# Optimization experiments

Hardware: AMD Instinct MI355X
Metric: run time of the kernel (lower is better)

Reference implementation:

```python
import jax, jax.numpy as jnp
import numpy as np

FEATURE_DIM = 2048
LABEL_DIM = 80
EMBED_DIM = 512
OUTPUT_DIM = 2048
NUM_EXPERTS = 8
BATCH = 1024
IN_DIM = FEATURE_DIM + EMBED_DIM


def setup_inputs() -> dict:
    key = jax.random.key(0)
    ks = jax.random.split(key, 7)
    features = jax.random.normal(ks[0], (BATCH, FEATURE_DIM), dtype=jnp.float32)
    labels = jax.random.uniform(ks[1], (BATCH, LABEL_DIM), dtype=jnp.float32)
    # learned parameters
    label_embed = jax.random.normal(ks[2], (LABEL_DIM, EMBED_DIM), dtype=jnp.float32)
    gate_w = jax.random.normal(ks[3], (IN_DIM, NUM_EXPERTS), dtype=jnp.float32) * (1.0 / np.sqrt(IN_DIM))
    gate_b = jnp.zeros((NUM_EXPERTS,), dtype=jnp.float32)
    expert_w = jax.random.normal(ks[4], (NUM_EXPERTS, IN_DIM, OUTPUT_DIM), dtype=jnp.float32) * (1.0 / np.sqrt(IN_DIM))
    expert_b = jnp.zeros((NUM_EXPERTS, OUTPUT_DIM), dtype=jnp.float32)
    return {
        "features": features,
        "labels": labels,
        "label_embed": label_embed,
        "gate_w": gate_w,
        "gate_b": gate_b,
        "expert_w": expert_w,
        "expert_b": expert_b,
    }


def reference(features, labels, label_embed, gate_w, gate_b, expert_w, expert_b):
    # labels: [B, L] soft multilabel -> label embedding mix [B, E]
    label_embeds = labels @ label_embed                      # [B, EMBED_DIM]
    combined = jnp.concatenate([features, label_embeds], axis=-1)  # [B, IN_DIM]
    gating = jax.nn.sigmoid(combined @ gate_w + gate_b)      # [B, NUM_EXPERTS]
    # all-experts batched GEMM: [B, IN] x [E, IN, OUT] -> [B, E, OUT]
    expert_out = jnp.einsum('bi,eio->beo', combined, expert_w) + expert_b[None, :, :]
    # gate-weighted reduction over experts
    out = jnp.einsum('be,beo->bo', gating, expert_out)       # [B, OUT]
    return out
```

## Files before the change

kernel.cpp:

```cpp
#include <hip/hip_runtime.h>
#include <hip/hip_bf16.h>

#define BATCH   1024
#define FDIM    2048
#define LDIM    80
#define EDIM    512
#define ODIM    2048
#define NEXP    8
#define INDIM   2560

#define BM      256
#define BN      256
#define BK      64
#define NKT     (INDIM / BK)

typedef __bf16 bf16x8 __attribute__((ext_vector_type(8)));
typedef float  f32x4  __attribute__((ext_vector_type(4)));

__device__ __forceinline__ unsigned int pack2(float lo, float hi) {
    __hip_bfloat162 h = __float22bfloat162_rn(make_float2(lo, hi));
    unsigned int u;
    __builtin_memcpy(&u, &h, 4);
    return u;
}
__device__ __forceinline__ float bf2f(unsigned short h) {
    return __uint_as_float((unsigned int)h << 16);
}
__device__ __forceinline__ void gload_lds16(const void* g, void* l) {
    __builtin_amdgcn_global_load_lds(
        (__attribute__((address_space(1))) void*)g,
        (__attribute__((address_space(3))) void*)l,
        16, 0, 0);
}

#define BAR()       __builtin_amdgcn_s_barrier()
#define SCHED_PIN() __builtin_amdgcn_sched_barrier(0)

__global__ __launch_bounds__(256) void convert_w(
    const float* __restrict__ W, unsigned short* __restrict__ Wb)
{
    const int t  = threadIdx.x;
    const int o  = blockIdx.x * 256 + t;
    const int k0 = blockIdx.y * 32;
    const int e  = blockIdx.z;
    const float* src = W + (size_t)e * ((size_t)INDIM * ODIM) + (size_t)k0 * ODIM + o;
    unsigned int pk[16];
    #pragma unroll
    for (int j = 0; j < 16; ++j) {
        float a = src[(size_t)(2 * j) * ODIM];
        float b = src[(size_t)(2 * j + 1) * ODIM];
        pk[j] = pack2(a, b);
    }
    uint4* dst = (uint4*)(Wb + (size_t)e * ((size_t)ODIM * INDIM) + (size_t)o * INDIM + k0);
    dst[0] = make_uint4(pk[0],  pk[1],  pk[2],  pk[3]);
    dst[1] = make_uint4(pk[4],  pk[5],  pk[6],  pk[7]);
    dst[2] = make_uint4(pk[8],  pk[9],  pk[10], pk[11]);
    dst[3] = make_uint4(pk[12], pk[13], pk[14], pk[15]);
}

__global__ __launch_bounds__(256) void prep_kernel(
    const float* __restrict__ features, const float* __restrict__ labels,
    const float* __restrict__ label_embed, unsigned short* __restrict__ cb)
{
    const int b0 = blockIdx.x * 4;
    const int t  = threadIdx.x;
    __shared__ float lab[4][LDIM];
    for (int idx = t; idx < 4 * LDIM; idx += 256) {
        lab[idx / LDIM][idx % LDIM] = labels[(size_t)(b0 + idx / LDIM) * LDIM + (idx % LDIM)];
    }
    __syncthreads();

    {
        const int r = t >> 6, c64 = t & 63;
        const float4* F4 = (const float4*)features;
        #pragma unroll
        for (int ch = 0; ch < 8; ++ch) {
            float4 v = F4[(size_t)(b0 + r) * (FDIM / 4) + c64 + 64 * ch];
            uint2 pk;
            pk.x = pack2(v.x, v.y);
            pk.y = pack2(v.z, v.w);
            *(uint2*)(cb + (size_t)(b0 + r) * INDIM + (size_t)(c64 + 64 * ch) * 4) = pk;
        }
    }
    {
        const int j = 2 * t;
        float acc[4][2] = {{0,0},{0,0},{0,0},{0,0}};
        const float2* le2 = (const float2*)label_embed;
        for (int l = 0; l < LDIM; ++l) {
            float2 le = le2[(size_t)l * (EDIM / 2) + t];
            #pragma unroll
            for (int r = 0; r < 4; ++r) {
                float lv = lab[r][l];
                acc[r][0] += lv * le.x;
                acc[r][1] += lv * le.y;
            }
        }
        #pragma unroll
        for (int r = 0; r < 4; ++r) {
            *(unsigned int*)(cb + (size_t)(b0 + r) * INDIM + FDIM + j) = pack2(acc[r][0], acc[r][1]);
        }
    }
}

__global__ __launch_bounds__(256) void gate_kernel(
    const unsigned short* __restrict__ cb, const float* __restrict__ gw,
    const float* __restrict__ gb, float* __restrict__ gating)
{
    const int b = blockIdx.x, t = threadIdx.x;
    float p[NEXP] = {0,0,0,0,0,0,0,0};
    for (int i = t; i < INDIM; i += 256) {
        float c = bf2f(cb[(size_t)b * INDIM + i]);
        const float4* g4 = (const float4*)(gw + (size_t)i * NEXP);
        float4 u = g4[0], v = g4[1];
        p[0] += c * u.x; p[1] += c * u.y; p[2] += c * u.z; p[3] += c * u.w;
        p[4] += c * v.x; p[5] += c * v.y; p[6] += c * v.z; p[7] += c * v.w;
    }
    __shared__ float red[4][NEXP];
    const int lane = t & 63, wave = t >> 6;
    #pragma unroll
    for (int e = 0; e < NEXP; ++e) {
        float v = p[e];
        v += __shfl_down(v, 32); v += __shfl_down(v, 16); v += __shfl_down(v, 8);
        v += __shfl_down(v, 4);  v += __shfl_down(v, 2);  v += __shfl_down(v, 1);
        if (lane == 0) red[wave][e] = v;
    }
    __syncthreads();
    if (t < NEXP) {
        float s = red[0][t] + red[1][t] + red[2][t] + red[3][t] + gb[t];
        gating[(size_t)b * NEXP + t] = 1.0f / (1.0f + __expf(-s));
    }
}

__global__ __launch_bounds__(512, 2) void moe_gemm8(
    const unsigned short* __restrict__ cb, const unsigned short* __restrict__ Wb,
    const float* __restrict__ gating, const float* __restrict__ eb,
    float* __restrict__ out)
{
    __shared__ unsigned short smem[2 * 2 * 256 * 64];

    const int t = threadIdx.x;
    const int lane = t & 63, wave = t >> 6;
    const int n0 = blockIdx.x * BN;
    const int m0 = blockIdx.y * BM;
    const int e  = blockIdx.z;

    const int wmi = wave >> 2;
    const int wni = wave & 3;
    const int wmBase = wmi * 128;
    const int wnBase = wni * 64;
    const int fm = lane & 15, fq = lane >> 4;
    const int fsw = fm & 7;

    const int srow = t >> 3;
    const int scn  = (t & 7) ^ (srow & 7);
    const size_t gOff = (size_t)srow * INDIM + (size_t)scn * 8;
    const unsigned short* aS = cb + (size_t)m0 * INDIM + gOff;
    const unsigned short* bS = Wb + (size_t)e * ((size_t)ODIM * INDIM)
                                  + (size_t)n0 * INDIM + gOff;

    #define STAGE_A(p, q, kt) gload_lds16(aS + (size_t)(q) * (64 * INDIM) + (size_t)(kt) * 64, \
            smem + (((p) * 2 + 0) * 256 + (q) * 64) * 64 + wave * 512)
    #define STAGE_B(p, q, kt) gload_lds16(bS + (size_t)(q) * (64 * INDIM) + (size_t)(kt) * 64, \
            smem + (((p) * 2 + 1) * 256 + (q) * 64) * 64 + wave * 512)

    f32x4 acc[8][4];
    #pragma unroll
    for (int i = 0; i < 8; ++i)
        #pragma unroll
        for (int j = 0; j < 4; ++j) acc[i][j] = (f32x4){0.f, 0.f, 0.f, 0.f};

    bf16x8 af[4][2], bA[2][2], bB[2][2];

    STAGE_A(0, 0, 0); STAGE_A(0, 2, 0); STAGE_B(0, 0, 0); STAGE_B(0, 1, 0);
    STAGE_B(0, 2, 0); STAGE_B(0, 3, 0); STAGE_A(0, 1, 0); STAGE_A(0, 3, 0);
    STAGE_A(1, 0, 1); STAGE_A(1, 2, 1); STAGE_B(1, 0, 1); STAGE_B(1, 1, 1);
    STAGE_B(1, 2, 1); STAGE_B(1, 3, 1);
    asm volatile("s_waitcnt vmcnt(6)");
    BAR();

    for (int kt = 0; kt < NKT; ++kt) {
        const int p  = kt & 1;
        const int np = p ^ 1;
        const unsigned short* Ac = smem + (p * 2 + 0) * (256 * 64);
        const unsigned short* Bc = smem + (p * 2 + 1) * (256 * 64);

        #pragma unroll
        for (int mi = 0; mi < 4; ++mi)
            #pragma unroll
            for (int ks = 0; ks < 2; ++ks)
                af[mi][ks] = *(const bf16x8*)(Ac + (wmBase + mi * 16 + fm) * 64
                                                 + (((ks * 4 + fq) ^ fsw) * 8));
        #pragma unroll
        for (int ni = 0; ni < 2; ++ni)
            #pragma unroll
            for (int ks = 0; ks < 2; ++ks)
                bA[ni][ks] = *(const bf16x8*)(Bc + (wnBase + ni * 16 + fm) * 64
                                                 + (((ks * 4 + fq) ^ fsw) * 8));
        if (kt + 1 < NKT) { STAGE_A(np, 1, kt + 1); STAGE_A(np, 3, kt + 1); }
        BAR();
        __builtin_amdgcn_s_setprio(1);
        #pragma unroll
        for (int mi = 0; mi < 4; ++mi)
            #pragma unroll
            for (int ni = 0; ni < 2; ++ni)
                #pragma unroll
                for (int ks = 0; ks < 2; ++ks)
                    acc[mi][ni] = __builtin_amdgcn_mfma_f32_16x16x32_bf16(
                        af[mi][ks], bA[ni][ks], acc[mi][ni], 0, 0, 0);
        __builtin_amdgcn_s_setprio(0);
        SCHED_PIN();
        BAR();

        #pragma unroll
        for (int ni = 0; ni < 2; ++ni)
            #pragma unroll
            for (int ks = 0; ks < 2; ++ks)
                bB[ni][ks] = *(const bf16x8*)(Bc + (wnBase + (2 + ni) * 16 + fm) * 64
                                                 + (((ks * 4 + fq) ^ fsw) * 8));
        if (kt + 2 < NKT) { STAGE_A(p, 0, kt + 2); STAGE_A(p, 2, kt + 2); }
        BAR();
        __builtin_amdgcn_s_setprio(1);
        #pragma unroll
        for (int mi = 0; mi < 4; ++mi)
            #pragma unroll
            for (int ni = 0; ni < 2; ++ni)
                #pragma unroll
                for (int ks = 0; ks < 2; ++ks)
                    acc[mi][2 + ni] = __builtin_amdgcn_mfma_f32_16x16x32_bf16(
                        af[mi][ks], bB[ni][ks], acc[mi][2 + ni], 0, 0, 0);
        __builtin_amdgcn_s_setprio(0);
        SCHED_PIN();
        BAR();

        #pragma unroll
        for (int mi = 0; mi < 4; ++mi)
            #pragma unroll
            for (int ks = 0; ks < 2; ++ks)
                af[mi][ks] = *(const bf16x8*)(Ac + (wmBase + 64 + mi * 16 + fm) * 64
                                                 + (((ks * 4 + fq) ^ fsw) * 8));
        if (kt + 2 < NKT) { STAGE_B(p, 0, kt + 2); STAGE_B(p, 1, kt + 2); }
        BAR();
        __builtin_amdgcn_s_setprio(1);
        #pragma unroll
        for (int mi = 0; mi < 4; ++mi)
            #pragma unroll
            for (int ni = 0; ni < 2; ++ni)
                #pragma unroll
                for (int ks = 0; ks < 2; ++ks)
                    acc[4 + mi][2 + ni] = __builtin_amdgcn_mfma_f32_16x16x32_bf16(
                        af[mi][ks], bB[ni][ks], acc[4 + mi][2 + ni], 0, 0, 0);
        __builtin_amdgcn_s_setprio(0);
        SCHED_PIN();
        BAR();

        if (kt + 2 < NKT) { STAGE_B(p, 2, kt + 2); STAGE_B(p, 3, kt + 2); }
        BAR();
        __builtin_amdgcn_s_setprio(1);
        #pragma unroll
        for (int mi = 0; mi < 4; ++mi)
            #pragma unroll
            for (int ni = 0; ni < 2; ++ni)
                #pragma unroll
                for (int ks = 0; ks < 2; ++ks)
                    acc[4 + mi][ni] = __builtin_amdgcn_mfma_f32_16x16x32_bf16(
                        af[mi][ks], bA[ni][ks], acc[4 + mi][ni], 0, 0, 0);
        __builtin_amdgcn_s_setprio(0);
        SCHED_PIN();
        if (kt + 2 < NKT) { asm volatile("s_waitcnt vmcnt(6)"); }
        else              { asm volatile("s_waitcnt vmcnt(0)"); }
        BAR();
    }
    #undef STAGE_A
    #undef STAGE_B

    #pragma unroll
    for (int mi = 0; mi < 8; ++mi) {
        const int grow = m0 + wmBase + mi * 16 + fq * 4;
        const float g0 = gating[(size_t)(grow + 0) * NEXP + e];
        const float g1 = gating[(size_t)(grow + 1) * NEXP + e];
        const float g2 = gating[(size_t)(grow + 2) * NEXP + e];
        const float g3 = gating[(size_t)(grow + 3) * NEXP + e];
        #pragma unroll
        for (int ni = 0; ni < 4; ++ni) {
            const int gcol = n0 + wnBase + ni * 16 + fm;
            const float bias = eb[(size_t)e * ODIM + gcol];
            f32x4 a = acc[mi][ni];
            unsafeAtomicAdd(out + (size_t)(grow + 0) * ODIM + gcol, g0 * (a.x + bias));
            unsafeAtomicAdd(out + (size_t)(grow + 1) * ODIM + gcol, g1 * (a.y + bias));
            unsafeAtomicAdd(out + (size_t)(grow + 2) * ODIM + gcol, g2 * (a.z + bias));
            unsafeAtomicAdd(out + (size_t)(grow + 3) * ODIM + gcol, g3 * (a.w + bias));
        }
    }
}

__global__ __launch_bounds__(256) void moe_gemm_slow(
    const unsigned short* __restrict__ cb, const float* __restrict__ W,
    const float* __restrict__ gating, const float* __restrict__ eb,
    float* __restrict__ out)
{
    __shared__ unsigned short As[128 * 32];
    __shared__ unsigned short Bs[128 * 32];

    const int t = threadIdx.x;
    const int lane = t & 63, wave = t >> 6;
    const int n0 = blockIdx.x * 128;
    const int m0 = blockIdx.y * 128;
    const int e  = blockIdx.z;

    f32x4 acc[4][4];
    #pragma unroll
    for (int i = 0; i < 4; ++i)
        #pragma unroll
        for (int j = 0; j < 4; ++j) acc[i][j] = (f32x4){0.f, 0.f, 0.f, 0.f};

    const int arow = t >> 2, acg = t & 3;
    const unsigned short* ag0 = cb + (size_t)(m0 + arow) * INDIM + acg * 8;
    unsigned short* al0 = As + wave * 512;
    unsigned short* al1 = As + 2048 + wave * 512;

    const int bg = t & 15;
    const int bu = t >> 4;
    const float* wg = W + (size_t)e * ((size_t)INDIM * ODIM) + (size_t)(2 * bg) * ODIM + n0 + bu * 8;
    unsigned int* bl = (unsigned int*)Bs + bg + bu * 128;

    const int fm = lane & 15, fq = lane >> 4;
    const int wn = (wave & 1) * 64;
    const int wm = (wave >> 1) * 64;

    for (int k0 = 0; k0 < INDIM; k0 += 32) {
        __syncthreads();
        gload_lds16(ag0 + k0, al0);
        gload_lds16(ag0 + (size_t)64 * INDIM + k0, al1);
        const float* wp = wg + (size_t)k0 * ODIM;
        float4 r0a = *(const float4*)(wp);
        float4 r0b = *(const float4*)(wp + 4);
        float4 r1a = *(const float4*)(wp + ODIM);
        float4 r1b = *(const float4*)(wp + ODIM + 4);
        bl[0 * 16] = pack2(r0a.x, r1a.x);
        bl[1 * 16] = pack2(r0a.y, r1a.y);
        bl[2 * 16] = pack2(r0a.z, r1a.z);
        bl[3 * 16] = pack2(r0a.w, r1a.w);
        bl[4 * 16] = pack2(r0b.x, r1b.x);
        bl[5 * 16] = pack2(r0b.y, r1b.y);
        bl[6 * 16] = pack2(r0b.z, r1b.z);
        bl[7 * 16] = pack2(r0b.w, r1b.w);
        __syncthreads();

        bf16x8 af[4], bfr[4];
        #pragma unroll
        for (int mi = 0; mi < 4; ++mi)
            af[mi] = *(const bf16x8*)(As + (wm + mi * 16 + fm) * 32 + fq * 8);
        #pragma unroll
        for (int ni = 0; ni < 4; ++ni)
            bfr[ni] = *(const bf16x8*)(Bs + (wn + ni * 16 + fm) * 32 + fq * 8);
        #pragma unroll
        for (int mi = 0; mi < 4; ++mi)
            #pragma unroll
            for (int ni = 0; ni < 4; ++ni)
                acc[mi][ni] = __builtin_amdgcn_mfma_f32_16x16x32_bf16(af[mi], bfr[ni], acc[mi][ni], 0, 0, 0);
    }

    #pragma unroll
    for (int mi = 0; mi < 4; ++mi) {
        const int grow = m0 + wm + mi * 16 + fq * 4;
        const float g0 = gating[(size_t)(grow + 0) * NEXP + e];
        const float g1 = gating[(size_t)(grow + 1) * NEXP + e];
        const float g2 = gating[(size_t)(grow + 2) * NEXP + e];
        const float g3 = gating[(size_t)(grow + 3) * NEXP + e];
        #pragma unroll
        for (int ni = 0; ni < 4; ++ni) {
            const int gcol = n0 + wn + ni * 16 + fm;
            const float bias = eb[(size_t)e * ODIM + gcol];
            f32x4 a = acc[mi][ni];
            unsafeAtomicAdd(out + (size_t)(grow + 0) * ODIM + gcol, g0 * (a.x + bias));
            unsafeAtomicAdd(out + (size_t)(grow + 1) * ODIM + gcol, g1 * (a.y + bias));
            unsafeAtomicAdd(out + (size_t)(grow + 2) * ODIM + gcol, g2 * (a.z + bias));
            unsafeAtomicAdd(out + (size_t)(grow + 3) * ODIM + gcol, g3 * (a.w + bias));
        }
    }
}

extern "C" void kernel_launch(void* const* d_in, const int* in_sizes, int n_in,
                              void* d_out, int out_size, void* d_ws, size_t ws_size,
                              hipStream_t stream) {
    const float* features    = (const float*)d_in[0];
    const float* labels      = (const float*)d_in[1];
    const float* label_embed = (const float*)d_in[2];
    const float* gate_w      = (const float*)d_in[3];
    const float* gate_b      = (const float*)d_in[4];
    const float* expert_w    = (const float*)d_in[5];
    const float* expert_b    = (const float*)d_in[6];
    float* out = (float*)d_out;

    const size_t wb_bytes = (size_t)NEXP * ODIM * INDIM * 2;
    const size_t cb_bytes = (size_t)BATCH * INDIM * 2;
    const size_t gt_bytes = (size_t)BATCH * NEXP * 4;
    const bool fast = ws_size >= wb_bytes + cb_bytes + gt_bytes;

    hipMemsetAsync(d_out, 0, (size_t)BATCH * ODIM * sizeof(float), stream);

    if (fast) {
        unsigned short* Wb = (unsigned short*)d_ws;
        unsigned short* cb = (unsigned short*)((char*)d_ws + wb_bytes);
        float* gating = (float*)((char*)d_ws + wb_bytes + cb_bytes);
        convert_w<<<dim3(ODIM / 256, INDIM / 32, NEXP), 256, 0, stream>>>(expert_w, Wb);
        prep_kernel<<<BATCH / 4, 256, 0, stream>>>(features, labels, label_embed, cb);
        gate_kernel<<<BATCH, 256, 0, stream>>>(cb, gate_w, gate_b, gating);
        moe_gemm8<<<dim3(ODIM / BN, BATCH / BM, NEXP), 512, 0, stream>>>(cb, Wb, gating, expert_b, out);
    } else {
        unsigned short* cb = (unsigned short*)d_ws;
        float* gating = (float*)((char*)d_ws + cb_bytes);
        prep_kernel<<<BATCH / 4, 256, 0, stream>>>(features, labels, label_embed, cb);
        gate_kernel<<<BATCH, 256, 0, stream>>>(cb, gate_w, gate_b, gating);
        moe_gemm_slow<<<dim3(ODIM / 128, BATCH / 128, NEXP), 256, 0, stream>>>(cb, expert_w, gating, expert_b, out);
    }
}
```

Baseline: 426.8 us.

## Split LDS buffers and unroll the K loop by two with a reworked prefetch schedule

Replaces the single indexed shared-memory array with four named A/B ping-pong buffers. The K loop is unrolled by two so buffer selection happens at compile time instead of through runtime parity math. The prefetch schedule also changes: each tile now loads all of next tile's A in one burst at the start, and B two tiles ahead after the last B read, replacing the interleaved half-tile staging. The aim is less address arithmetic and simpler vmcnt accounting, at the risk of burstier global loads and different latency overlap.

```diff
diff --git a/kernel.cpp b/kernel.cpp
--- a/kernel.cpp
+++ b/kernel.cpp
@@ -136,7 +136,10 @@
     const float* __restrict__ gating, const float* __restrict__ eb,
     float* __restrict__ out)
 {
-    __shared__ unsigned short smem[2 * 2 * 256 * 64];
+    __shared__ unsigned short As0[256 * 64];
+    __shared__ unsigned short Bs0[256 * 64];
+    __shared__ unsigned short As1[256 * 64];
+    __shared__ unsigned short Bs1[256 * 64];
 
     const int t = threadIdx.x;
     const int lane = t & 63, wave = t >> 6;
@@ -158,10 +161,26 @@
     const unsigned short* bS = Wb + (size_t)e * ((size_t)ODIM * INDIM)
                                   + (size_t)n0 * INDIM + gOff;
 
-    #define STAGE_A(p, q, kt) gload_lds16(aS + (size_t)(q) * (64 * INDIM) + (size_t)(kt) * 64, \
-            smem + (((p) * 2 + 0) * 256 + (q) * 64) * 64 + wave * 512)
-    #define STAGE_B(p, q, kt) gload_lds16(bS + (size_t)(q) * (64 * INDIM) + (size_t)(kt) * 64, \
-            smem + (((p) * 2 + 1) * 256 + (q) * 64) * 64 + wave * 512)
+    #define STAGE4_A(DST, kt) { _Pragma("unroll") for (int q = 0; q < 4; ++q) \
+        gload_lds16(aS + (size_t)q * (64 * INDIM) + (size_t)(kt) * 64, (DST) + q * 4096 + wave * 512); }
+    #define STAGE4_B(DST, kt) { _Pragma("unroll") for (int q = 0; q < 4; ++q) \
+        gload_lds16(bS + (size_t)q * (64 * INDIM) + (size_t)(kt) * 64, (DST) + q * 4096 + wave * 512); }
+
+    #define PH_READ_A(RA, base) { _Pragma("unroll") for (int mi = 0; mi < 4; ++mi) \
+        _Pragma("unroll") for (int ks = 0; ks < 2; ++ks) \
+            af[mi][ks] = *(const bf16x8*)((RA) + (wmBase + (base) + mi * 16 + fm) * 64 \
+                                               + (((ks * 4 + fq) ^ fsw) * 8)); }
+    #define PH_READ_B(BF, RB, base) { _Pragma("unroll") for (int ni = 0; ni < 2; ++ni) \
+        _Pragma("unroll") for (int ks = 0; ks < 2; ++ks) \
+            BF[ni][ks] = *(const bf16x8*)((RB) + (wnBase + (base) + ni * 16 + fm) * 64 \
+                                               + (((ks * 4 + fq) ^ fsw) * 8)); }
+    #define MFMA16(AI, AJ, BF) { __builtin_amdgcn_s_setprio(1); \
+        _Pragma("unroll") for (int mi = 0; mi < 4; ++mi) \
+        _Pragma("unroll") for (int ni = 0; ni < 2; ++ni) \
+        _Pragma("unroll") for (int ks = 0; ks < 2; ++ks) \
+            acc[(AI) + mi][(AJ) + ni] = __builtin_amdgcn_mfma_f32_16x16x32_bf16( \
+                af[mi][ks], BF[ni][ks], acc[(AI) + mi][(AJ) + ni], 0, 0, 0); \
+        __builtin_amdgcn_s_setprio(0); }
 
     f32x4 acc[8][4];
     #pragma unroll
@@ -171,107 +190,48 @@
 
     bf16x8 af[4][2], bA[2][2], bB[2][2];
 
-    STAGE_A(0, 0, 0); STAGE_A(0, 2, 0); STAGE_B(0, 0, 0); STAGE_B(0, 1, 0);
-    STAGE_B(0, 2, 0); STAGE_B(0, 3, 0); STAGE_A(0, 1, 0); STAGE_A(0, 3, 0);
-    STAGE_A(1, 0, 1); STAGE_A(1, 2, 1); STAGE_B(1, 0, 1); STAGE_B(1, 1, 1);
-    STAGE_B(1, 2, 1); STAGE_B(1, 3, 1);
-    asm volatile("s_waitcnt vmcnt(6)");
-    BAR();
-
-    for (int kt = 0; kt < NKT; ++kt) {
-        const int p  = kt & 1;
-        const int np = p ^ 1;
-        const unsigned short* Ac = smem + (p * 2 + 0) * (256 * 64);
-        const unsigned short* Bc = smem + (p * 2 + 1) * (256 * 64);
-
-        #pragma unroll
-        for (int mi = 0; mi < 4; ++mi)
-            #pragma unroll
-            for (int ks = 0; ks < 2; ++ks)
-                af[mi][ks] = *(const bf16x8*)(Ac + (wmBase + mi * 16 + fm) * 64
-                                                 + (((ks * 4 + fq) ^ fsw) * 8));
-        #pragma unroll
-        for (int ni = 0; ni < 2; ++ni)
-            #pragma unroll
-            for (int ks = 0; ks < 2; ++ks)
-                bA[ni][ks] = *(const bf16x8*)(Bc + (wnBase + ni * 16 + fm) * 64
-                                                 + (((ks * 4 + fq) ^ fsw) * 8));
-        if (kt + 1 < NKT) { STAGE_A(np, 1, kt + 1); STAGE_A(np, 3, kt + 1); }
-        BAR();
-        __builtin_amdgcn_s_setprio(1);
-        #pragma unroll
-        for (int mi = 0; mi < 4; ++mi)
-            #pragma unroll
-            for (int ni = 0; ni < 2; ++ni)
-                #pragma unroll
-                for (int ks = 0; ks < 2; ++ks)
-                    acc[mi][ni] = __builtin_amdgcn_mfma_f32_16x16x32_bf16(
-                        af[mi][ks], bA[ni][ks], acc[mi][ni], 0, 0, 0);
-        __builtin_amdgcn_s_setprio(0);
-        SCHED_PIN();
-        BAR();
-
-        #pragma unroll
-        for (int ni = 0; ni < 2; ++ni)
-            #pragma unroll
-            for (int ks = 0; ks < 2; ++ks)
-                bB[ni][ks] = *(const bf16x8*)(Bc + (wnBase + (2 + ni) * 16 + fm) * 64
-                                                 + (((ks * 4 + fq) ^ fsw) * 8));
-        if (kt + 2 < NKT) { STAGE_A(p, 0, kt + 2); STAGE_A(p, 2, kt + 2); }
-        BAR();
-        __builtin_amdgcn_s_setprio(1);
-        #pragma unroll
-        for (int mi = 0; mi < 4; ++mi)
-            #pragma unroll
-            for (int ni = 0; ni < 2; ++ni)
-                #pragma unroll
-                for (int ks = 0; ks < 2; ++ks)
-                    acc[mi][2 + ni] = __builtin_amdgcn_mfma_f32_16x16x32_bf16(
-                        af[mi][ks], bB[ni][ks], acc[mi][2 + ni], 0, 0, 0);
-        __builtin_amdgcn_s_setprio(0);
-        SCHED_PIN();
-        BAR();
-
-        #pragma unroll
-        for (int mi = 0; mi < 4; ++mi)
-            #pragma unroll
-            for (int ks = 0; ks < 2; ++ks)
-                af[mi][ks] = *(const bf16x8*)(Ac + (wmBase + 64 + mi * 16 + fm) * 64
-                                                 + (((ks * 4 + fq) ^ fsw) * 8));
-        if (kt + 2 < NKT) { STAGE_B(p, 0, kt + 2); STAGE_B(p, 1, kt + 2); }
-        BAR();
-        __builtin_amdgcn_s_setprio(1);
-        #pragma unroll
-        for (int mi = 0; mi < 4; ++mi)
-            #pragma unroll
-            for (int ni = 0; ni < 2; ++ni)
-                #pragma unroll
-                for (int ks = 0; ks < 2; ++ks)
-                    acc[4 + mi][2 + ni] = __builtin_amdgcn_mfma_f32_16x16x32_bf16(
-                        af[mi][ks], bB[ni][ks], acc[4 + mi][2 + ni], 0, 0, 0);
-        __builtin_amdgcn_s_setprio(0);
-        SCHED_PIN();
-        BAR();
-
-        if (kt + 2 < NKT) { STAGE_B(p, 2, kt + 2); STAGE_B(p, 3, kt + 2); }
-        BAR();
-        __builtin_amdgcn_s_setprio(1);
-        #pragma unroll
-        for (int mi = 0; mi < 4; ++mi)
-            #pragma unroll
-            for (int ni = 0; ni < 2; ++ni)
-                #pragma unroll
-                for (int ks = 0; ks < 2; ++ks)
-                    acc[4 + mi][ni] = __builtin_amdgcn_mfma_f32_16x16x32_bf16(
-                        af[mi][ks], bA[ni][ks], acc[4 + mi][ni], 0, 0, 0);
-        __builtin_amdgcn_s_setprio(0);
-        SCHED_PIN();
-        if (kt + 2 < NKT) { asm volatile("s_waitcnt vmcnt(6)"); }
-        else              { asm volatile("s_waitcnt vmcnt(0)"); }
-        BAR();
-    }
-    #undef STAGE_A
-    #undef STAGE_B
+    STAGE4_A(As0, 0); STAGE4_B(Bs0, 0); STAGE4_B(Bs1, 1);
+    asm volatile("s_waitcnt vmcnt(4)");
+    BAR(); SCHED_PIN();
+
+    #define TILE(kt, RA, RB, OA) { \
+         \
+        PH_READ_A(RA, 0); \
+        PH_READ_B(bA, RB, 0); \
+        if ((kt) + 1 < NKT) STAGE4_A(OA, (kt) + 1); \
+        BAR(); \
+        MFMA16(0, 0, bA); \
+        SCHED_PIN(); BAR(); SCHED_PIN(); \
+         \
+        PH_READ_B(bB, RB, 32); \
+        BAR(); \
+        MFMA16(0, 2, bB); \
+        SCHED_PIN(); BAR(); SCHED_PIN(); \
+         \
+        PH_READ_A(RA, 64); \
+        BAR(); \
+        MFMA16(4, 2, bB); \
+        SCHED_PIN(); BAR(); SCHED_PIN(); \
+         \
+        if ((kt) + 2 < NKT) STAGE4_B(RB, (kt) + 2); \
+        BAR(); \
+        MFMA16(4, 0, bA); \
+        SCHED_PIN(); \
+        if ((kt) + 2 < NKT) { asm volatile("s_waitcnt vmcnt(4)"); } \
+        else                { asm volatile("s_waitcnt vmcnt(0)"); } \
+        BAR(); SCHED_PIN(); \
+    }
+
+    for (int kt = 0; kt < NKT; kt += 2) {
+        TILE(kt,     As0, Bs0, As1);
+        TILE(kt + 1, As1, Bs1, As0);
+    }
+    #undef TILE
+    #undef STAGE4_A
+    #undef STAGE4_B
+    #undef PH_READ_A
+    #undef PH_READ_B
+    #undef MFMA16
 
     #pragma unroll
     for (int mi = 0; mi < 8; ++mi) {
```

Result: slower. 437.7 us (+2.6%).
